# Performance work log

Measured on AMD Instinct MI355X. Metric: run time of the kernel, lower is better.

Reference implementation:

```python
import jax, jax.numpy as jnp
import numpy as np

N, E = 20000, 320000
IN, HID, OUT, H = 128, 32, 1, 4
EPS = 1e-16  # PyG softmax epsilon


def _p(key, shape, scale=0.05):
    return jax.random.normal(key, shape, dtype=jnp.float32) * scale


def setup_inputs() -> dict:
    key = jax.random.key(0)
    ks = jax.random.split(key, 20)
    d = {
        "x": jax.random.normal(ks[0], (N, IN), dtype=jnp.float32),
        "edge_src": jax.random.randint(ks[1], (E,), 0, N, dtype=jnp.int32),
        "edge_dst": jax.random.randint(ks[2], (E,), 0, N, dtype=jnp.int32),
        # layer 1: TransformerConv(IN, HID, H)  ->  [N, H*HID]
        "W1q": _p(ks[3], (IN, H * HID)), "b1q": jnp.zeros((H * HID,), jnp.float32),
        "W1k": _p(ks[4], (IN, H * HID)), "b1k": jnp.zeros((H * HID,), jnp.float32),
        "W1v": _p(ks[5], (IN, H * HID)), "b1v": jnp.zeros((H * HID,), jnp.float32),
        "W1s": _p(ks[6], (IN, H * HID)), "b1s": jnp.zeros((H * HID,), jnp.float32),
        # layer 2: TransformerConv(H*HID, OUT, H) -> [N, H*OUT]
        "W2q": _p(ks[7], (H * HID, H * OUT)), "b2q": jnp.zeros((H * OUT,), jnp.float32),
        "W2k": _p(ks[8], (H * HID, H * OUT)), "b2k": jnp.zeros((H * OUT,), jnp.float32),
        "W2v": _p(ks[9], (H * HID, H * OUT)), "b2v": jnp.zeros((H * OUT,), jnp.float32),
        "W2s": _p(ks[10], (H * HID, H * OUT)), "b2s": jnp.zeros((H * OUT,), jnp.float32),
        # final nn.Linear(heads, 1)
        "Wl": _p(ks[11], (H, 1)), "bl": jnp.zeros((1,), jnp.float32),
    }
    return d


def transformer_conv(x, src, dst, Wq, bq, Wk, bk, Wv, bv, Ws, bs, heads, ch):
    n = x.shape[0]
    q = (x @ Wq + bq).reshape(n, heads, ch)
    k = (x @ Wk + bk).reshape(n, heads, ch)
    v = (x @ Wv + bv).reshape(n, heads, ch)
    qi, kj, vj = q[dst], k[src], v[src]            # [E,H,C] gathers
    score = (qi * kj).sum(-1) / jnp.sqrt(jnp.float32(ch))  # [E,H]
    m = jax.ops.segment_max(score, dst, num_segments=n)    # segment softmax by target
    e = jnp.exp(score - m[dst])
    s = jax.ops.segment_sum(e, dst, num_segments=n)
    alpha = e / (s[dst] + EPS)                              # [E,H]
    agg = jax.ops.segment_sum(alpha[:, :, None] * vj, dst, num_segments=n)  # [N,H,C]
    return agg.reshape(n, heads * ch) + x @ Ws + bs          # concat + root skip


def reference(x, edge_src, edge_dst,
              W1q, b1q, W1k, b1k, W1v, b1v, W1s, b1s,
              W2q, b2q, W2k, b2k, W2v, b2v, W2s, b2s,
              Wl, bl):
    h = transformer_conv(x, edge_src, edge_dst, W1q, b1q, W1k, b1k, W1v, b1v, W1s, b1s, H, HID)
    h = jax.nn.relu(h)  # dropout is identity in eval
    h = transformer_conv(h, edge_src, edge_dst, W2q, b2q, W2k, b2k, W2v, b2v, W2s, b2s, H, OUT)
    y = h @ Wl + bl                      # [N,1]
    return y.mean(axis=0, keepdims=True)  # [1,1]
```

## Files before the change

### kernel.cpp

```cpp
#include <hip/hip_runtime.h>
#include <math.h>

static constexpr float EPS_PYG = 1e-16f;
static constexpr float INV_SQRT32 = 0.17677669529663687f;
static constexpr int CAP = 64;
static constexpr int CAP_SH = 6;

typedef short bf16x8 __attribute__((ext_vector_type(8)));
typedef float f32x4 __attribute__((ext_vector_type(4)));

__device__ inline unsigned short f2bf(float f) {
    union { float f; unsigned u; } x; x.f = f;
    unsigned r = x.u + 0x7FFFu + ((x.u >> 16) & 1u);
    return (unsigned short)(r >> 16);
}
__device__ inline float bf_hi(unsigned u) {
    union { unsigned u; float f; } x; x.u = u & 0xFFFF0000u; return x.f;
}
__device__ inline float bf_lo(unsigned u) {
    union { unsigned u; float f; } x; x.u = u << 16; return x.f;
}

__global__ __launch_bounds__(256) void build_csr_kernel(
    const int* __restrict__ src, const int* __restrict__ dst,
    int* __restrict__ deg, int* __restrict__ csr_src,
    int E, int nblk_deg,
    const float* __restrict__ Wq, const float* __restrict__ Wk,
    const float* __restrict__ Wv, const float* __restrict__ Wsk,
    unsigned short* __restrict__ Wbt,
    float* __restrict__ out, const float* __restrict__ bl)
{
    const int b = blockIdx.x;
    const int t = threadIdx.x;
    if (b < nblk_deg) {
        int e = b * 256 + t;
        if (e < E) {
            int d = dst[e];
            int s = atomicAdd(&deg[d], 1);
            if (s < CAP) csr_src[(d << CAP_SH) + s] = src[e];
        }
    } else if (b < nblk_deg + 4) {
        int m = b - nblk_deg;
        const float* W = (m == 0) ? Wq : (m == 1) ? Wk : (m == 2) ? Wv : Wsk;
        for (int i = t; i < 16384; i += 256) {
            int k = i >> 7, nn = i & 127;
            Wbt[(m << 14) + nn * 128 + k] = f2bf(W[i]);
        }
    } else {
        if (t == 0) out[0] = bl[0];
    }
}

__global__ __launch_bounds__(256) void gemm1_mfma(
    const float* __restrict__ X, const unsigned short* __restrict__ Wbt,
    const float* __restrict__ bq, const float* __restrict__ bk,
    const float* __restrict__ bv, const float* __restrict__ bsk,
    unsigned int* __restrict__ QS, unsigned int* __restrict__ KV, int n)
{
    const int tid  = threadIdx.x;
    const int wave = tid >> 6;
    const int lane = tid & 63;
    const int m    = lane & 15;
    const int quad = lane >> 4;
    const int r0   = blockIdx.x * 64 + wave * 16;

    int arow = r0 + m;
    if (arow >= n) arow = n - 1;

    const float4* xr = (const float4*)(X + (size_t)arow * 128);

    bf16x8 afr[4];
#pragma unroll
    for (int kc4 = 0; kc4 < 4; ++kc4) {
        float4 f0 = xr[kc4 * 8 + quad * 2];
        float4 f1 = xr[kc4 * 8 + quad * 2 + 1];
        bf16x8 a;
        a[0] = (short)f2bf(f0.x); a[1] = (short)f2bf(f0.y);
        a[2] = (short)f2bf(f0.z); a[3] = (short)f2bf(f0.w);
        a[4] = (short)f2bf(f1.x); a[5] = (short)f2bf(f1.y);
        a[6] = (short)f2bf(f1.z); a[7] = (short)f2bf(f1.w);
        afr[kc4] = a;
    }

#pragma unroll
    for (int mode = 0; mode < 2; ++mode) {
        const unsigned short* WA = Wbt + (size_t)(mode ? 1 : 0) * 16384;
        const unsigned short* WB = Wbt + (size_t)(mode ? 2 : 3) * 16384;
        const float* biasA = mode ? bk : bq;
        const float* biasB = mode ? bv : bsk;
        unsigned int* Out = mode ? KV : QS;

        f32x4 accA[8] = {};
        f32x4 accB[8] = {};
#pragma unroll
        for (int kc4 = 0; kc4 < 4; ++kc4) {
            const int koff = kc4 * 32 + quad * 8;
#pragma unroll
            for (int ct = 0; ct < 8; ++ct) {
                bf16x8 ba = *(const bf16x8*)(WA + (ct * 16 + m) * 128 + koff);
                accA[ct] = __builtin_amdgcn_mfma_f32_16x16x32_bf16(afr[kc4], ba, accA[ct], 0, 0, 0);
                bf16x8 bb = *(const bf16x8*)(WB + (ct * 16 + m) * 128 + koff);
                accB[ct] = __builtin_amdgcn_mfma_f32_16x16x32_bf16(afr[kc4], bb, accB[ct], 0, 0, 0);
            }
        }
#pragma unroll
        for (int ct = 0; ct < 8; ++ct) {
            const int col = ct * 16 + m;
            const float bA = biasA[col], bB = biasB[col];
#pragma unroll
            for (int r = 0; r < 4; ++r) {
                const int row = r0 + quad * 4 + r;
                if (row < n) {
                    unsigned ha = f2bf(accA[ct][r] + bA);
                    unsigned lb = f2bf(accB[ct][r] + bB);
                    Out[(size_t)row * 128 + col] = (ha << 16) | lb;
                }
            }
        }
    }
}

__global__ __launch_bounds__(256) void l1_agg_kernel(
    const unsigned int* __restrict__ QS, const unsigned int* __restrict__ KV,
    const int* __restrict__ deg, const int* __restrict__ csr_src,
    const float* __restrict__ W2q, const float* __restrict__ W2k,
    const float* __restrict__ W2v, const float* __restrict__ W2s,
    const float* __restrict__ b2q, const float* __restrict__ b2k,
    const float* __restrict__ b2v, const float* __restrict__ b2s,
    float4* __restrict__ Q2, float4* __restrict__ KV2, float4* __restrict__ S2,
    int n)
{
    const int t = threadIdx.x;
    const int node = blockIdx.x * 4 + (t >> 6);
    if (node >= n) return;
    const int l    = t & 31;
    const int half = (t >> 5) & 1;
    const int lf   = t & 63;
    const int cbase = ((l >> 3) << 5) + ((l & 7) << 2);

    const int beg = node << CAP_SH;
    int cnt = deg[node]; if (cnt > CAP) cnt = CAP;

    const int eall = csr_src[beg + lf];

    const uint4 qs = *(const uint4*)(QS + (size_t)node * 128 + cbase);
    const float4 q = make_float4(bf_hi(qs.x), bf_hi(qs.y), bf_hi(qs.z), bf_hi(qs.w));

    float lsum = 0.f, a0 = 0.f, a1 = 0.f, a2 = 0.f, a3 = 0.f;
    int p_base = 0;
    for (; p_base + 8 <= cnt; p_base += 8) {
        const int p = p_base + half;
        int s0 = __shfl(eall, p, 64);
        int s1 = __shfl(eall, p + 2, 64);
        int s2 = __shfl(eall, p + 4, 64);
        int s3 = __shfl(eall, p + 6, 64);
        uint4 u0 = *(const uint4*)(KV + (size_t)s0 * 128 + cbase);
        uint4 u1 = *(const uint4*)(KV + (size_t)s1 * 128 + cbase);
        uint4 u2 = *(const uint4*)(KV + (size_t)s2 * 128 + cbase);
        uint4 u3 = *(const uint4*)(KV + (size_t)s3 * 128 + cbase);
        float p0 = q.x * bf_hi(u0.x) + q.y * bf_hi(u0.y)
                 + q.z * bf_hi(u0.z) + q.w * bf_hi(u0.w);
        float p1 = q.x * bf_hi(u1.x) + q.y * bf_hi(u1.y)
                 + q.z * bf_hi(u1.z) + q.w * bf_hi(u1.w);
        float p2 = q.x * bf_hi(u2.x) + q.y * bf_hi(u2.y)
                 + q.z * bf_hi(u2.z) + q.w * bf_hi(u2.w);
        float p3 = q.x * bf_hi(u3.x) + q.y * bf_hi(u3.y)
                 + q.z * bf_hi(u3.z) + q.w * bf_hi(u3.w);
        p0 += __shfl_xor(p0, 4, 8);  p1 += __shfl_xor(p1, 4, 8);
        p2 += __shfl_xor(p2, 4, 8);  p3 += __shfl_xor(p3, 4, 8);
        p0 += __shfl_xor(p0, 2, 8);  p1 += __shfl_xor(p1, 2, 8);
        p2 += __shfl_xor(p2, 2, 8);  p3 += __shfl_xor(p3, 2, 8);
        p0 += __shfl_xor(p0, 1, 8);  p1 += __shfl_xor(p1, 1, 8);
        p2 += __shfl_xor(p2, 1, 8);  p3 += __shfl_xor(p3, 1, 8);
        float e0 = __expf(p0 * INV_SQRT32);
        float e1 = __expf(p1 * INV_SQRT32);
        float e2 = __expf(p2 * INV_SQRT32);
        float e3 = __expf(p3 * INV_SQRT32);
        lsum += (e0 + e1) + (e2 + e3);
        a0 += e0 * bf_lo(u0.x) + e1 * bf_lo(u1.x)
            + e2 * bf_lo(u2.x) + e3 * bf_lo(u3.x);
        a1 += e0 * bf_lo(u0.y) + e1 * bf_lo(u1.y)
            + e2 * bf_lo(u2.y) + e3 * bf_lo(u3.y);
        a2 += e0 * bf_lo(u0.z) + e1 * bf_lo(u1.z)
            + e2 * bf_lo(u2.z) + e3 * bf_lo(u3.z);
        a3 += e0 * bf_lo(u0.w) + e1 * bf_lo(u1.w)
            + e2 * bf_lo(u2.w) + e3 * bf_lo(u3.w);
    }
    if (p_base < cnt) {
        const int pclamp = cnt - 1;
#pragma unroll
        for (int j = 0; j < 4; ++j) {
            int p = p_base + half + 2 * j;
            const bool valid = p < cnt;
            int ps = valid ? p : pclamp;
            int s0 = __shfl(eall, ps, 64);
            uint4 u0 = *(const uint4*)(KV + (size_t)s0 * 128 + cbase);
            float p0 = q.x * bf_hi(u0.x) + q.y * bf_hi(u0.y)
                     + q.z * bf_hi(u0.z) + q.w * bf_hi(u0.w);
            p0 += __shfl_xor(p0, 4, 8);
            p0 += __shfl_xor(p0, 2, 8);
            p0 += __shfl_xor(p0, 1, 8);
            float e0 = valid ? __expf(p0 * INV_SQRT32) : 0.f;
            lsum += e0;
            a0 += e0 * bf_lo(u0.x);
            a1 += e0 * bf_lo(u0.y);
            a2 += e0 * bf_lo(u0.z);
            a3 += e0 * bf_lo(u0.w);
        }
    }
    lsum += __shfl_xor(lsum, 32, 64);
    a0   += __shfl_xor(a0,   32, 64);
    a1   += __shfl_xor(a1,   32, 64);
    a2   += __shfl_xor(a2,   32, 64);
    a3   += __shfl_xor(a3,   32, 64);

    const float inv = 1.0f / (lsum + EPS_PYG);
    const float h0 = fmaxf(a0 * inv + bf_lo(qs.x), 0.f);
    const float h1 = fmaxf(a1 * inv + bf_lo(qs.y), 0.f);
    const float h2 = fmaxf(a2 * inv + bf_lo(qs.z), 0.f);
    const float h3 = fmaxf(a3 * inv + bf_lo(qs.w), 0.f);

    const float* WA = half ? W2v : W2q;
    const float* WB = half ? W2s : W2k;
    float p0, p1, p2, p3, p4, p5, p6, p7;
    {
        float4 wa = *(const float4*)(WA + (size_t)(cbase + 0) * 4);
        float4 wb = *(const float4*)(WB + (size_t)(cbase + 0) * 4);
        p0 = h0 * wa.x; p1 = h0 * wa.y; p2 = h0 * wa.z; p3 = h0 * wa.w;
        p4 = h0 * wb.x; p5 = h0 * wb.y; p6 = h0 * wb.z; p7 = h0 * wb.w;
        wa = *(const float4*)(WA + (size_t)(cbase + 1) * 4);
        wb = *(const float4*)(WB + (size_t)(cbase + 1) * 4);
        p0 += h1 * wa.x; p1 += h1 * wa.y; p2 += h1 * wa.z; p3 += h1 * wa.w;
        p4 += h1 * wb.x; p5 += h1 * wb.y; p6 += h1 * wb.z; p7 += h1 * wb.w;
        wa = *(const float4*)(WA + (size_t)(cbase + 2) * 4);
        wb = *(const float4*)(WB + (size_t)(cbase + 2) * 4);
        p0 += h2 * wa.x; p1 += h2 * wa.y; p2 += h2 * wa.z; p3 += h2 * wa.w;
        p4 += h2 * wb.x; p5 += h2 * wb.y; p6 += h2 * wb.z; p7 += h2 * wb.w;
        wa = *(const float4*)(WA + (size_t)(cbase + 3) * 4);
        wb = *(const float4*)(WB + (size_t)(cbase + 3) * 4);
        p0 += h3 * wa.x; p1 += h3 * wa.y; p2 += h3 * wa.z; p3 += h3 * wa.w;
        p4 += h3 * wb.x; p5 += h3 * wb.y; p6 += h3 * wb.z; p7 += h3 * wb.w;
    }
#pragma unroll
    for (int mk = 16; mk >= 1; mk >>= 1) {
        p0 += __shfl_xor(p0, mk, 32); p1 += __shfl_xor(p1, mk, 32);
        p2 += __shfl_xor(p2, mk, 32); p3 += __shfl_xor(p3, mk, 32);
        p4 += __shfl_xor(p4, mk, 32); p5 += __shfl_xor(p5, mk, 32);
        p6 += __shfl_xor(p6, mk, 32); p7 += __shfl_xor(p7, mk, 32);
    }
    if (lf == 0) {
        const float4 ba = *(const float4*)b2q;
        const float4 bb = *(const float4*)b2k;
        Q2[node] = make_float4(p0 + ba.x, p1 + ba.y, p2 + ba.z, p3 + ba.w);
        KV2[(size_t)node * 2 + 0] =
            make_float4(p4 + bb.x, p5 + bb.y, p6 + bb.z, p7 + bb.w);
    } else if (lf == 32) {
        const float4 ba = *(const float4*)b2v;
        const float4 bb = *(const float4*)b2s;
        KV2[(size_t)node * 2 + 1] =
            make_float4(p0 + ba.x, p1 + ba.y, p2 + ba.z, p3 + ba.w);
        S2[node] = make_float4(p4 + bb.x, p5 + bb.y, p6 + bb.z, p7 + bb.w);
    }
}

__global__ __launch_bounds__(256) void l2_agg_kernel(
    const float4* __restrict__ Q2, const float4* __restrict__ KV2,
    const float4* __restrict__ S2,
    const int* __restrict__ deg, const int* __restrict__ csr_src,
    const float* __restrict__ Wl, float* __restrict__ out, int n, float invn)
{
    const int t  = threadIdx.x;
    const int g  = t >> 4;
    const int gl = t & 15;
    const int nd = blockIdx.x * 16 + g;
    float y = 0.f;
    if (nd < n) {
        const int beg = nd << CAP_SH;
        int cnt = deg[nd]; if (cnt > CAP) cnt = CAP;
        const int end = beg + cnt;
        float4 q = Q2[nd];
        float l0 = 0.f, l1 = 0.f, l2 = 0.f, l3 = 0.f;
        float a0 = 0.f, a1 = 0.f, a2 = 0.f, a3 = 0.f;
        for (int pos = beg + gl; pos < end; pos += 16) {
            int src = csr_src[pos];
            float4 k = KV2[(size_t)src * 2 + 0];
            float4 v = KV2[(size_t)src * 2 + 1];
            float e0 = __expf(q.x * k.x);
            float e1 = __expf(q.y * k.y);
            float e2 = __expf(q.z * k.z);
            float e3 = __expf(q.w * k.w);
            l0 += e0; a0 += e0 * v.x;
            l1 += e1; a1 += e1 * v.y;
            l2 += e2; a2 += e2 * v.z;
            l3 += e3; a3 += e3 * v.w;
        }
#pragma unroll
        for (int mk = 8; mk >= 1; mk >>= 1) {
            l0 += __shfl_xor(l0, mk, 16); l1 += __shfl_xor(l1, mk, 16);
            l2 += __shfl_xor(l2, mk, 16); l3 += __shfl_xor(l3, mk, 16);
            a0 += __shfl_xor(a0, mk, 16); a1 += __shfl_xor(a1, mk, 16);
            a2 += __shfl_xor(a2, mk, 16); a3 += __shfl_xor(a3, mk, 16);
        }
        if (gl == 0) {
            float4 sk = S2[nd];
            float h0 = a0 / (l0 + EPS_PYG) + sk.x;
            float h1 = a1 / (l1 + EPS_PYG) + sk.y;
            float h2 = a2 / (l2 + EPS_PYG) + sk.z;
            float h3 = a3 / (l3 + EPS_PYG) + sk.w;
            y = (h0 * Wl[0] + h1 * Wl[1] + h2 * Wl[2] + h3 * Wl[3]) * invn;
        }
    }
    __shared__ float red[256];
    red[t] = y;
    __syncthreads();
    for (int off = 128; off > 0; off >>= 1) {
        if (t < (unsigned)off) red[t] += red[t + off];
        __syncthreads();
    }
    if (t == 0) atomicAdd(out, red[0]);
}

extern "C" void kernel_launch(void* const* d_in, const int* in_sizes, int n_in,
                              void* d_out, int out_size, void* d_ws, size_t ws_size,
                              hipStream_t stream) {
    const float* x        = (const float*)d_in[0];
    const int*   edge_src = (const int*)d_in[1];
    const int*   edge_dst = (const int*)d_in[2];
    const float* W1q = (const float*)d_in[3];  const float* b1q = (const float*)d_in[4];
    const float* W1k = (const float*)d_in[5];  const float* b1k = (const float*)d_in[6];
    const float* W1v = (const float*)d_in[7];  const float* b1v = (const float*)d_in[8];
    const float* W1s = (const float*)d_in[9];  const float* b1s = (const float*)d_in[10];
    const float* W2q = (const float*)d_in[11]; const float* b2q = (const float*)d_in[12];
    const float* W2k = (const float*)d_in[13]; const float* b2k = (const float*)d_in[14];
    const float* W2v = (const float*)d_in[15]; const float* b2v = (const float*)d_in[16];
    const float* W2s = (const float*)d_in[17]; const float* b2s = (const float*)d_in[18];
    const float* Wl  = (const float*)d_in[19]; const float* bl  = (const float*)d_in[20];

    const int N = in_sizes[0] / 128;
    const int E = in_sizes[1];
    float* out = (float*)d_out;

    float* ws  = (float*)d_ws;
    size_t off = 0;
    unsigned int* QS  = (unsigned int*)(ws + off); off += (size_t)N * 128;
    unsigned int* KV  = (unsigned int*)(ws + off); off += (size_t)N * 128;
    float*        q2  = ws + off; off += (size_t)N * 4;
    float*        kv2 = ws + off; off += (size_t)N * 8;
    float*        s2  = ws + off; off += (size_t)N * 4;
    unsigned short* Wbt = (unsigned short*)(ws + off); off += 4 * 16384 / 2;
    int* deg     = (int*)(ws + off);
    int* csr_src = deg + N;

    const int nblk_e = (E + 255) / 256;
    const int nblk_g = (N + 63) / 64;

    hipMemsetAsync(deg, 0, (size_t)N * sizeof(int), stream);
    build_csr_kernel<<<nblk_e + 5, 256, 0, stream>>>(
        edge_src, edge_dst, deg, csr_src, E, nblk_e,
        W1q, W1k, W1v, W1s, Wbt, out, bl);
    gemm1_mfma<<<nblk_g, 256, 0, stream>>>(x, Wbt, b1q, b1k, b1v, b1s,
                                           QS, KV, N);
    l1_agg_kernel<<<(N + 3) / 4, 256, 0, stream>>>(
        QS, KV, deg, csr_src, W2q, W2k, W2v, W2s, b2q, b2k, b2v, b2s,
        (float4*)q2, (float4*)kv2, (float4*)s2, N);
    l2_agg_kernel<<<(N + 15) / 16, 256, 0, stream>>>((const float4*)q2,
                                                     (const float4*)kv2,
                                                     (const float4*)s2,
                                                     deg, csr_src, Wl, out, N,
                                                     1.0f / (float)N);
}
```

Before: 218.4 us.

## Split layer-1 GEMM over a 2D grid and batch four edges per CSR thread

The layer-1 MFMA GEMM now launches a 2D grid whose y dimension selects the projection pair (Q/skip or K/V) and the column half, so each block computes a quarter of the outputs with fewer accumulators. This is meant to raise occupancy and parallelism for a grid that was previously only about 313 blocks. Every block still re-reads its X rows and redoes the bf16 conversion, so that work is repeated four times. Separately, CSR construction now has each thread handle four edges, issuing all loads and then all atomics together so more memory traffic is in flight per thread.

```diff
diff --git a/kernel.cpp b/kernel.cpp
--- a/kernel.cpp
+++ b/kernel.cpp
@@ -33,12 +33,24 @@
     const int b = blockIdx.x;
     const int t = threadIdx.x;
     if (b < nblk_deg) {
-        int e = b * 256 + t;
-        if (e < E) {
-            int d = dst[e];
-            int s = atomicAdd(&deg[d], 1);
-            if (s < CAP) csr_src[(d << CAP_SH) + s] = src[e];
-        }
+        const int e0 = b * 1024 + t;
+        const int e1 = e0 + 256, e2 = e0 + 512, e3 = e0 + 768;
+        const bool v0 = e0 < E, v1 = e1 < E, v2 = e2 < E, v3 = e3 < E;
+        int d0 = 0, d1 = 0, d2 = 0, d3 = 0;
+        int s0 = 0, s1 = 0, s2 = 0, s3 = 0;
+        if (v0) { d0 = dst[e0]; s0 = src[e0]; }
+        if (v1) { d1 = dst[e1]; s1 = src[e1]; }
+        if (v2) { d2 = dst[e2]; s2 = src[e2]; }
+        if (v3) { d3 = dst[e3]; s3 = src[e3]; }
+        int sl0 = 0, sl1 = 0, sl2 = 0, sl3 = 0;
+        if (v0) sl0 = atomicAdd(&deg[d0], 1);
+        if (v1) sl1 = atomicAdd(&deg[d1], 1);
+        if (v2) sl2 = atomicAdd(&deg[d2], 1);
+        if (v3) sl3 = atomicAdd(&deg[d3], 1);
+        if (v0 && sl0 < CAP) csr_src[(d0 << CAP_SH) + sl0] = s0;
+        if (v1 && sl1 < CAP) csr_src[(d1 << CAP_SH) + sl1] = s1;
+        if (v2 && sl2 < CAP) csr_src[(d2 << CAP_SH) + sl2] = s2;
+        if (v3 && sl3 < CAP) csr_src[(d3 << CAP_SH) + sl3] = s3;
     } else if (b < nblk_deg + 4) {
         int m = b - nblk_deg;
         const float* W = (m == 0) ? Wq : (m == 1) ? Wk : (m == 2) ? Wv : Wsk;
@@ -57,6 +69,9 @@
     const float* __restrict__ bv, const float* __restrict__ bsk,
     unsigned int* __restrict__ QS, unsigned int* __restrict__ KV, int n)
 {
+    const int mode  = blockIdx.y >> 1;
+    const int chalf = blockIdx.y & 1;
+
     const int tid  = threadIdx.x;
     const int wave = tid >> 6;
     const int lane = tid & 63;
@@ -82,39 +97,37 @@
         afr[kc4] = a;
     }
 
-#pragma unroll
-    for (int mode = 0; mode < 2; ++mode) {
-        const unsigned short* WA = Wbt + (size_t)(mode ? 1 : 0) * 16384;
-        const unsigned short* WB = Wbt + (size_t)(mode ? 2 : 3) * 16384;
-        const float* biasA = mode ? bk : bq;
-        const float* biasB = mode ? bv : bsk;
-        unsigned int* Out = mode ? KV : QS;
-
-        f32x4 accA[8] = {};
-        f32x4 accB[8] = {};
-#pragma unroll
-        for (int kc4 = 0; kc4 < 4; ++kc4) {
-            const int koff = kc4 * 32 + quad * 8;
-#pragma unroll
-            for (int ct = 0; ct < 8; ++ct) {
-                bf16x8 ba = *(const bf16x8*)(WA + (ct * 16 + m) * 128 + koff);
-                accA[ct] = __builtin_amdgcn_mfma_f32_16x16x32_bf16(afr[kc4], ba, accA[ct], 0, 0, 0);
-                bf16x8 bb = *(const bf16x8*)(WB + (ct * 16 + m) * 128 + koff);
-                accB[ct] = __builtin_amdgcn_mfma_f32_16x16x32_bf16(afr[kc4], bb, accB[ct], 0, 0, 0);
-            }
-        }
-#pragma unroll
-        for (int ct = 0; ct < 8; ++ct) {
-            const int col = ct * 16 + m;
-            const float bA = biasA[col], bB = biasB[col];
-#pragma unroll
-            for (int r = 0; r < 4; ++r) {
-                const int row = r0 + quad * 4 + r;
-                if (row < n) {
-                    unsigned ha = f2bf(accA[ct][r] + bA);
-                    unsigned lb = f2bf(accB[ct][r] + bB);
-                    Out[(size_t)row * 128 + col] = (ha << 16) | lb;
-                }
+    const unsigned short* WA = Wbt + (size_t)(mode ? 1 : 0) * 16384;
+    const unsigned short* WB = Wbt + (size_t)(mode ? 2 : 3) * 16384;
+    const float* biasA = mode ? bk : bq;
+    const float* biasB = mode ? bv : bsk;
+    unsigned int* Out = mode ? KV : QS;
+
+    f32x4 accA[4] = {};
+    f32x4 accB[4] = {};
+#pragma unroll
+    for (int kc4 = 0; kc4 < 4; ++kc4) {
+        const int koff = kc4 * 32 + quad * 8;
+#pragma unroll
+        for (int c = 0; c < 4; ++c) {
+            const int ct = chalf * 4 + c;
+            bf16x8 ba = *(const bf16x8*)(WA + (ct * 16 + m) * 128 + koff);
+            accA[c] = __builtin_amdgcn_mfma_f32_16x16x32_bf16(afr[kc4], ba, accA[c], 0, 0, 0);
+            bf16x8 bb = *(const bf16x8*)(WB + (ct * 16 + m) * 128 + koff);
+            accB[c] = __builtin_amdgcn_mfma_f32_16x16x32_bf16(afr[kc4], bb, accB[c], 0, 0, 0);
+        }
+    }
+#pragma unroll
+    for (int c = 0; c < 4; ++c) {
+        const int col = (chalf * 4 + c) * 16 + m;
+        const float bA = biasA[col], bB = biasB[col];
+#pragma unroll
+        for (int r = 0; r < 4; ++r) {
+            const int row = r0 + quad * 4 + r;
+            if (row < n) {
+                unsigned ha = f2bf(accA[c][r] + bA);
+                unsigned lb = f2bf(accB[c][r] + bB);
+                Out[(size_t)row * 128 + col] = (ha << 16) | lb;
             }
         }
     }
@@ -351,15 +364,18 @@
     int* deg     = (int*)(ws + off);
     int* csr_src = deg + N;
 
-    const int nblk_e = (E + 255) / 256;
-    const int nblk_g = (N + 63) / 64;
+    const int nblk_e4 = (E + 1023) / 1024;
+    const int nblk_g  = (N + 63) / 64;
 
     hipMemsetAsync(deg, 0, (size_t)N * sizeof(int), stream);
-    build_csr_kernel<<<nblk_e + 5, 256, 0, stream>>>(
-        edge_src, edge_dst, deg, csr_src, E, nblk_e,
+    build_csr_kernel<<<nblk_e4 + 5, 256, 0, stream>>>(
+        edge_src, edge_dst, deg, csr_src, E, nblk_e4,
         W1q, W1k, W1v, W1s, Wbt, out, bl);
-    gemm1_mfma<<<nblk_g, 256, 0, stream>>>(x, Wbt, b1q, b1k, b1v, b1s,
-                                           QS, KV, N);
+    {
+        dim3 grid(nblk_g, 4);
+        gemm1_mfma<<<grid, 256, 0, stream>>>(x, Wbt, b1q, b1k, b1v, b1s,
+                                             QS, KV, N);
+    }
     l1_agg_kernel<<<(N + 3) / 4, 256, 0, stream>>>(
         QS, KV, deg, csr_src, W2q, W2k, W2v, W2s, b2q, b2k, b2v, b2s,
         (float4*)q2, (float4*)kv2, (float4*)s2, N);
```

After: 208.7 us. 4.4% less time.
